# Optimization experiments

Measured on AMD Instinct MI355X. Metric: run time of the kernel, lower is better.

Reference implementation:

```python
import jax, jax.numpy as jnp
import numpy as np

H, DK = 16, 64
F = H * DK  # n_feat = 1024
B, T = 2, 2048


def setup_inputs() -> dict:
    key = jax.random.key(0)
    ks = jax.random.split(key, 11)
    mk = lambda k, sh: jax.random.normal(k, sh, dtype=jnp.float32)
    inp = {
        "query": mk(ks[0], (B, T, F)),
        "key": mk(ks[1], (B, T, F)),
        "value": mk(ks[2], (B, T, F)),
    }
    # Standard RoPE frequency table, shaped [T,1,1,DK] to broadcast over [t,b,h,d].
    pos = jnp.arange(T, dtype=jnp.float32)[:, None]
    inv_freq = 1.0 / (10000.0 ** (jnp.arange(0, DK, 2, dtype=jnp.float32) / DK))
    ang = pos * inv_freq                       # [T, DK/2]
    emb = jnp.concatenate([ang, ang], axis=-1)  # [T, DK]
    inp["cos"] = jnp.cos(emb)[:, None, None, :]
    inp["sin"] = jnp.sin(emb)[:, None, None, :]
    scale = 1.0 / np.sqrt(F).astype(np.float32)
    for i, n in enumerate(["wq", "wk", "wv", "wo"]):
        inp[n] = mk(ks[3 + i], (F, F)) * scale  # torch Linear weight layout [out,in]
    for i, n in enumerate(["bq", "bk", "bv", "bo"]):
        inp[n] = mk(ks[7 + i], (F,)) * 0.01
    return inp


def _rtt_half(x):
    d = x.shape[-1]
    return jnp.concatenate([-x[..., d // 2:], x[..., :d // 2]], axis=-1)


def reference(query, key, value, cos, sin, wq, bq, wk, bk, wv, bv, wo, bo):
    b, t, f = query.shape
    h, d = H, DK
    # [b,t,f] -> [t,b,h,d] as in the torch code (RoPE applied pre-projection)
    to_tbhd = lambda x: jnp.swapaxes(x, 0, 1).reshape(t, b, h, d)
    q = to_tbhd(query)
    k = to_tbhd(key)
    c, s = cos[:t], sin[:t]
    q = q * c + _rtt_half(q) * s
    k = k * c + _rtt_half(k) * s
    back = lambda x: jnp.swapaxes(x.reshape(t, b, f), 0, 1)  # -> [b,t,f]
    q, k = back(q), back(k)
    lin = lambda x, w, bias: x @ w.T + bias
    Q = lin(q, wq, bq).reshape(b, t, h, d)
    K = lin(k, wk, bk).reshape(b, t, h, d)
    V = lin(value, wv, bv).reshape(b, t, h, d)
    scores = jnp.einsum('bqhd,bkhd->bhqk', Q, K) / jnp.sqrt(jnp.float32(d))
    attn = jax.nn.softmax(scores, axis=-1)
    o = jnp.einsum('bhqk,bkhd->bqhd', attn, V).reshape(b, t, f)
    return o @ wo.T + bo
```

## Files before the change

kernel.cpp:

```cpp
#include <hip/hip_runtime.h>
#include <hip/hip_bf16.h>

#define DEVI __device__ __forceinline__

typedef unsigned short u16;
typedef unsigned int u32;
typedef __attribute__((ext_vector_type(8))) short bf16x8;
typedef __attribute__((ext_vector_type(4))) short bf16x4;
typedef __attribute__((ext_vector_type(4))) float f32x4;

#define Bn 2
#define Tn 2048
#define Hn 16
#define Dn 64
#define Fn 1024

DEVI u16 tobf(float f) {
    __hip_bfloat16 h = __float2bfloat16(f);
    return __builtin_bit_cast(u16, h);
}
DEVI float frombf(u16 u) {
    return __builtin_bit_cast(float, ((u32)u) << 16);
}

DEVI f32x4 mfma16(bf16x8 a, bf16x8 b, f32x4 c) {
    return __builtin_amdgcn_mfma_f32_16x16x32_bf16(a, b, c, 0, 0, 0);
}

DEVI void gload_lds16(const u16* g, u16* l) {
    __builtin_amdgcn_global_load_lds(
        (const __attribute__((address_space(1))) void*)g,
        (__attribute__((address_space(3))) void*)l, 16, 0, 0);
}

__global__ __launch_bounds__(256) void k_prep(const float* __restrict__ q,
                                              const float* __restrict__ k,
                                              const float* __restrict__ v,
                                              const float* __restrict__ cosb,
                                              const float* __restrict__ sinb,
                                              const float* __restrict__ wq,
                                              const float* __restrict__ wk,
                                              const float* __restrict__ wv,
                                              const float* __restrict__ wo,
                                              u16* __restrict__ Aq,
                                              u16* __restrict__ Ak,
                                              u16* __restrict__ Av) {
    if (blockIdx.x < 4096) {
        unsigned idx = blockIdx.x * 256 + threadIdx.x;
        unsigned which = idx >> 19;
        unsigned r = idx & 0x7FFFFu;
        unsigned d0 = (r & 7u) << 2;
        unsigned h = (r >> 3) & 15u;
        unsigned t = (r >> 7) & 2047u;
        unsigned b = (r >> 18) & 1u;
        const float* src = which ? k : q;
        u16* dst = which ? Ak : Aq;
        size_t base = ((size_t)(b * Tn + t)) * Fn + h * Dn;
        float4 lo = *(const float4*)(src + base + d0);
        float4 hi = *(const float4*)(src + base + d0 + 32);
        float4 cl = *(const float4*)(cosb + (size_t)t * Dn + d0);
        float4 ch = *(const float4*)(cosb + (size_t)t * Dn + d0 + 32);
        float4 sl = *(const float4*)(sinb + (size_t)t * Dn + d0);
        float4 sh = *(const float4*)(sinb + (size_t)t * Dn + d0 + 32);
        bf16x4 olo, ohi;
        olo[0] = (short)tobf(lo.x * cl.x - hi.x * sl.x);
        olo[1] = (short)tobf(lo.y * cl.y - hi.y * sl.y);
        olo[2] = (short)tobf(lo.z * cl.z - hi.z * sl.z);
        olo[3] = (short)tobf(lo.w * cl.w - hi.w * sl.w);
        ohi[0] = (short)tobf(hi.x * ch.x + lo.x * sh.x);
        ohi[1] = (short)tobf(hi.y * ch.y + lo.y * sh.y);
        ohi[2] = (short)tobf(hi.z * ch.z + lo.z * sh.z);
        ohi[3] = (short)tobf(hi.w * ch.w + lo.w * sh.w);
        *(bf16x4*)(dst + base + d0) = olo;
        *(bf16x4*)(dst + base + d0 + 32) = ohi;
    } else {
        size_t i8 = (((size_t)blockIdx.x - 4096) * 256 + threadIdx.x) * 8;
        const size_t M4 = (size_t)4 << 20, M1 = (size_t)1 << 20;
        const float* src;
        size_t off;
        if (i8 < M4)              { src = v;  off = i8; }
        else if (i8 < M4 + M1)    { src = wq; off = i8 - M4; }
        else if (i8 < M4 + 2*M1)  { src = wk; off = i8 - M4 - M1; }
        else if (i8 < M4 + 3*M1)  { src = wv; off = i8 - M4 - 2*M1; }
        else                      { src = wo; off = i8 - M4 - 3*M1; }
        float4 a = *(const float4*)(src + off);
        float4 c = *(const float4*)(src + off + 4);
        bf16x8 vv;
        vv[0] = (short)tobf(a.x); vv[1] = (short)tobf(a.y);
        vv[2] = (short)tobf(a.z); vv[3] = (short)tobf(a.w);
        vv[4] = (short)tobf(c.x); vv[5] = (short)tobf(c.y);
        vv[6] = (short)tobf(c.z); vv[7] = (short)tobf(c.w);
        *(bf16x8*)(Av + i8) = vv;
    }
}

DEVI void store_out(u16* p, float v) { *p = tobf(v); }
DEVI void store_out(float* p, float v) { *p = v; }

template <typename OUT>
DEVI void gemm_body(const u16* __restrict__ A, const u16* __restrict__ W,
                    const float* __restrict__ bias, OUT* __restrict__ C,
                    float scale, u16* As, u16* Bs, int mode) {
    const int tid = threadIdx.x;
    const int lane = tid & 63;
    const int wave = tid >> 6;
    const int l15 = lane & 15, l4 = lane >> 4;
    const int id = blockIdx.x + (blockIdx.y << 3);
    const int swz = ((id & 7) << 5) + (id >> 3);
    const int bn = (swz & 7) << 7, bm = (swz >> 3) << 7;
    const int wr = (wave >> 1) << 6, wc = (wave & 1) << 6;

    const int c0 = tid, c1 = tid + 256;
    const u16* A0p = A + (size_t)(bm + (c0 >> 2)) * 1024 + ((c0 & 3) << 3);
    const u16* A1p = A + (size_t)(bm + (c1 >> 2)) * 1024 + ((c1 & 3) << 3);
    const u16* B0p = W + (size_t)(bn + (c0 >> 2)) * 1024 + ((c0 & 3) << 3);
    const u16* B1p = W + (size_t)(bn + (c1 >> 2)) * 1024 + ((c1 & 3) << 3);
    u16* Ad0 = As + (c0 << 3);
    u16* Ad1 = As + (c1 << 3);
    u16* Bd0 = Bs + (c0 << 3);
    u16* Bd1 = Bs + (c1 << 3);

    f32x4 acc[4][4] = {};

    for (int k0 = 0; k0 < 1024; k0 += 32) {
        gload_lds16(A0p + k0, Ad0);
        gload_lds16(A1p + k0, Ad1);
        gload_lds16(B0p + k0, Bd0);
        gload_lds16(B1p + k0, Bd1);
        __syncthreads();
        bf16x8 af[4], bfr[4];
        #pragma unroll
        for (int m = 0; m < 4; m++)
            af[m] = *(const bf16x8*)(As + (wr + m * 16 + l15) * 32 + (l4 << 3));
        #pragma unroll
        for (int n = 0; n < 4; n++)
            bfr[n] = *(const bf16x8*)(Bs + (wc + n * 16 + l15) * 32 + (l4 << 3));
        #pragma unroll
        for (int m = 0; m < 4; m++)
            #pragma unroll
            for (int n = 0; n < 4; n++)
                acc[m][n] = mfma16(af[m], bfr[n], acc[m][n]);
        __syncthreads();
    }

    #pragma unroll
    for (int m = 0; m < 4; m++)
        #pragma unroll
        for (int n = 0; n < 4; n++) {
            const int gcol = bn + wc + n * 16 + l15;
            const float bb = bias[gcol];
            #pragma unroll
            for (int j = 0; j < 4; j++) {
                const int grow = bm + wr + m * 16 + (l4 << 2) + j;
                const float val = (acc[m][n][j] + bb) * scale;
                if (mode == 0) {
                    store_out(C + (size_t)grow * 1024 + gcol, val);
                } else {
                    const int b = grow >> 11, t = grow & 2047;
                    const int h = gcol >> 6, d = gcol & 63;
                    const int bh = b * 16 + h, tt2 = t >> 6, r = t & 63;
                    const size_t tbase = ((size_t)(bh * 32 + tt2)) << 12;
                    size_t off;
                    if (mode == 1) {
                        const int nn = ((r >> 5) << 1) | ((r >> 2) & 1);
                        const int kk = d >> 5, ll4 = (d >> 3) & 3, e = d & 7;
                        const int ll15 = (((r >> 3) & 3) << 2) | (r & 3);
                        off = tbase + ((size_t)(nn * 2 + kk) << 9) +
                              ((ll4 * 16 + ll15) << 3) + e;
                    } else {
                        const int kk = r >> 5, ll4 = (r >> 3) & 3, e = r & 7;
                        const int nd = d >> 4, ll15 = d & 15;
                        off = tbase + ((size_t)(kk * 4 + nd) << 9) +
                              ((ll4 * 16 + ll15) << 3) + e;
                    }
                    ((u16*)C)[off] = tobf(val);
                }
            }
        }
}

__global__ __launch_bounds__(256) void k_gemm_qkv(
    const u16* A0, const u16* W0, const float* b0, u16* C0,
    const u16* A1, const u16* W1, const float* b1, u16* C1,
    const u16* A2, const u16* W2, const float* b2, u16* C2) {
    __shared__ __align__(16) u16 As[128 * 32];
    __shared__ __align__(16) u16 Bs[128 * 32];
    const int z = blockIdx.z;
    const u16* A = z == 0 ? A0 : (z == 1 ? A1 : A2);
    const u16* W = z == 0 ? W0 : (z == 1 ? W1 : W2);
    const float* bias = z == 0 ? b0 : (z == 1 ? b1 : b2);
    u16* C = z == 0 ? C0 : (z == 1 ? C1 : C2);
    const float scale = z == 0 ? 0.125f * 1.4426950408889634f : 1.0f;
    gemm_body<u16>(A, W, bias, C, scale, As, Bs, z);
}

__global__ __launch_bounds__(256) void k_gemm_f32(const u16* __restrict__ A,
                                                  const u16* __restrict__ W,
                                                  const float* __restrict__ bias,
                                                  float* __restrict__ C) {
    __shared__ __align__(16) u16 As[128 * 32];
    __shared__ __align__(16) u16 Bs[128 * 32];
    gemm_body<float>(A, W, bias, C, 1.0f, As, Bs, 0);
}

__global__ __launch_bounds__(256) void k_attn(const u16* __restrict__ Qp,
                                              const u16* __restrict__ Kr,
                                              const u16* __restrict__ Vr,
                                              u16* __restrict__ Op0,
                                              u16* __restrict__ Op1,
                                              float* __restrict__ Ls) {
    __shared__ __align__(16) u16 Ks[2][4096];
    __shared__ __align__(16) u16 Vs[2][4096];
    const int tid = threadIdx.x, wave = tid >> 6, lane = tid & 63;
    const int l15 = lane & 15, l4 = lane >> 4;
    const int bh = blockIdx.x, b = bh >> 4, h = bh & 15;
    const int sp = blockIdx.z;
    const int q0 = blockIdx.y * 128 + wave * 32;
    const int tbase = sp << 4;

    bf16x8 aq[2][2];
    #pragma unroll
    for (int mq = 0; mq < 2; mq++)
        #pragma unroll
        for (int kk = 0; kk < 2; kk++)
            aq[mq][kk] = *(const bf16x8*)(Qp +
                ((size_t)(b * Tn + q0 + mq * 16 + l15)) * Fn + h * Dn + kk * 32 + (l4 << 3));

    f32x4 o[2][4] = {};
    f32x4 osum[2] = {};
    const f32x4 zero4 = {0.f, 0.f, 0.f, 0.f};

    bf16x8 ones;
    #pragma unroll
    for (int j = 0; j < 8; j++) ones[j] = (short)0x3F80;

    const u16* Kbr = Kr + ((size_t)bh << 17);
    const u16* Vbr = Vr + ((size_t)bh << 17);
    const int lo8 = lane * 8;

    #define STAGE(bf, tg)                                                     \
        _Pragma("unroll")                                                     \
        for (int i = 0; i < 2; i++) {                                         \
            const int c = wave + i * 4;                                       \
            gload_lds16(Kbr + (((tg) * 8 + c) << 9) + lo8,                    \
                        &Ks[bf][(c << 9) + lo8]);                             \
            gload_lds16(Vbr + (((tg) * 8 + c) << 9) + lo8,                    \
                        &Vs[bf][(c << 9) + lo8]);                             \
        }

    STAGE(0, tbase);
    __syncthreads();
    int cur = 0;

    #pragma unroll 1
    for (int tt = 0; tt < 16; tt++) {
        if (tt < 15) STAGE(cur ^ 1, tbase + tt + 1);

        bf16x8 ka[4][2], va[2][4];
        #pragma unroll
        for (int n = 0; n < 4; n++)
            #pragma unroll
            for (int kk = 0; kk < 2; kk++)
                ka[n][kk] = *(const bf16x8*)(&Ks[cur][((n * 2 + kk) << 9) + lo8]);
        #pragma unroll
        for (int kk = 0; kk < 2; kk++)
            #pragma unroll
            for (int nd = 0; nd < 4; nd++)
                va[kk][nd] = *(const bf16x8*)(&Vs[cur][((kk * 4 + nd) << 9) + lo8]);

        f32x4 s[2][4];
        __builtin_amdgcn_s_setprio(1);
        #pragma unroll
        for (int n = 0; n < 4; n++) {
            s[0][n] = mfma16(ka[n][0], aq[0][0], zero4);
            s[1][n] = mfma16(ka[n][0], aq[1][0], zero4);
            s[0][n] = mfma16(ka[n][1], aq[0][1], s[0][n]);
            s[1][n] = mfma16(ka[n][1], aq[1][1], s[1][n]);
        }
        __builtin_amdgcn_s_setprio(0);

        bf16x8 pb[2][2];
        #pragma unroll
        for (int mq = 0; mq < 2; mq++)
            #pragma unroll
            for (int kk = 0; kk < 2; kk++) {
                float p0 = __builtin_amdgcn_exp2f(s[mq][2 * kk][0]);
                float p1 = __builtin_amdgcn_exp2f(s[mq][2 * kk][1]);
                float p2 = __builtin_amdgcn_exp2f(s[mq][2 * kk][2]);
                float p3 = __builtin_amdgcn_exp2f(s[mq][2 * kk][3]);
                float p4 = __builtin_amdgcn_exp2f(s[mq][2 * kk + 1][0]);
                float p5 = __builtin_amdgcn_exp2f(s[mq][2 * kk + 1][1]);
                float p6 = __builtin_amdgcn_exp2f(s[mq][2 * kk + 1][2]);
                float p7 = __builtin_amdgcn_exp2f(s[mq][2 * kk + 1][3]);
                bf16x8 pv;
                pv[0] = (short)tobf(p0); pv[1] = (short)tobf(p1);
                pv[2] = (short)tobf(p2); pv[3] = (short)tobf(p3);
                pv[4] = (short)tobf(p4); pv[5] = (short)tobf(p5);
                pv[6] = (short)tobf(p6); pv[7] = (short)tobf(p7);
                pb[mq][kk] = pv;
            }

        __builtin_amdgcn_s_setprio(1);
        osum[0] = mfma16(ones, pb[0][0], osum[0]);
        osum[1] = mfma16(ones, pb[1][0], osum[1]);
        osum[0] = mfma16(ones, pb[0][1], osum[0]);
        osum[1] = mfma16(ones, pb[1][1], osum[1]);
        #pragma unroll
        for (int kk = 0; kk < 2; kk++)
            #pragma unroll
            for (int nd = 0; nd < 4; nd++) {
                o[0][nd] = mfma16(va[kk][nd], pb[0][kk], o[0][nd]);
                o[1][nd] = mfma16(va[kk][nd], pb[1][kk], o[1][nd]);
            }
        __builtin_amdgcn_s_setprio(0);

        __syncthreads();
        cur ^= 1;
    }
    #undef STAGE

    u16* OpS = sp ? Op1 : Op0;
    #pragma unroll
    for (int mq = 0; mq < 2; mq++) {
        const int q = q0 + mq * 16 + l15;
        const float lsum = osum[mq][0];
        float inv = 1.f / lsum;
        #pragma unroll
        for (int nd = 0; nd < 4; nd++) {
            bf16x4 ov;
            ov[0] = (short)tobf(o[mq][nd][0] * inv);
            ov[1] = (short)tobf(o[mq][nd][1] * inv);
            ov[2] = (short)tobf(o[mq][nd][2] * inv);
            ov[3] = (short)tobf(o[mq][nd][3] * inv);
            *(bf16x4*)(OpS + ((size_t)(b * Tn + q)) * Fn +
                       h * Dn + nd * 16 + (l4 << 2)) = ov;
        }
        if (l4 == 0)
            Ls[(((size_t)(sp * 2 + b)) * Tn + q) * Hn + h] = lsum;
    }
}

__global__ __launch_bounds__(256) void k_combine(const u16* __restrict__ Op0,
                                                 const u16* __restrict__ Op1,
                                                 const float* __restrict__ Ls,
                                                 u16* __restrict__ Oa) {
    size_t e0 = ((size_t)blockIdx.x * 256 + threadIdx.x) * 8;
    int row = (int)(e0 >> 10);
    int b = row >> 11, q = row & 2047;
    int h = (int)(e0 >> 6) & 15;
    float l0 = Ls[(((size_t)(0 + b)) * Tn + q) * Hn + h];
    float l1 = Ls[(((size_t)(2 + b)) * Tn + q) * Hn + h];
    float inv = 1.f / (l0 + l1);
    float w0 = l0 * inv, w1 = l1 * inv;
    bf16x8 x0 = *(const bf16x8*)(Op0 + e0);
    bf16x8 x1 = *(const bf16x8*)(Op1 + e0);
    bf16x8 out;
    #pragma unroll
    for (int j = 0; j < 8; j++)
        out[j] = (short)tobf(frombf((u16)x0[j]) * w0 + frombf((u16)x1[j]) * w1);
    *(bf16x8*)(Oa + e0) = out;
}

extern "C" void kernel_launch(void* const* d_in, const int* in_sizes, int n_in,
                              void* d_out, int out_size, void* d_ws, size_t ws_size,
                              hipStream_t stream) {
    const float* q    = (const float*)d_in[0];
    const float* k    = (const float*)d_in[1];
    const float* v    = (const float*)d_in[2];
    const float* cosb = (const float*)d_in[3];
    const float* sinb = (const float*)d_in[4];
    const float* wq   = (const float*)d_in[5];
    const float* wk   = (const float*)d_in[6];
    const float* wv   = (const float*)d_in[7];
    const float* wo   = (const float*)d_in[8];
    const float* bq   = (const float*)d_in[9];
    const float* bk   = (const float*)d_in[10];
    const float* bv   = (const float*)d_in[11];
    const float* bo   = (const float*)d_in[12];

    char* ws = (char*)d_ws;
    char* dob = (char*)d_out;
    const size_t MB = (size_t)1 << 20;
    u16* Aq  = (u16*)(ws);
    u16* Ak  = (u16*)(ws + 8 * MB);
    u16* Av  = (u16*)(ws + 16 * MB);
    u16* Wq  = (u16*)(ws + 24 * MB);
    u16* Wk  = (u16*)(ws + 26 * MB);
    u16* Wv  = (u16*)(ws + 28 * MB);
    u16* Wo  = (u16*)(ws + 30 * MB);
    u16* Qp  = (u16*)(ws + 32 * MB);
    u16* Kr  = (u16*)(ws + 40 * MB);
    u16* Vr  = (u16*)(ws + 48 * MB);
    u16* Op0 = (u16*)(dob);
    u16* Op1 = (u16*)(dob + 8 * MB);
    float* Ls = (float*)(ws + 16 * MB);
    u16* Oa  = (u16*)(ws);

    k_prep<<<8192, 256, 0, stream>>>(q, k, v, cosb, sinb, wq, wk, wv, wo,
                                     Aq, Ak, Av);
    k_gemm_qkv<<<dim3(8, 32, 3), 256, 0, stream>>>(Aq, Wq, bq, Qp,
                                                   Ak, Wk, bk, Kr,
                                                   Av, Wv, bv, Vr);
    k_attn<<<dim3(32, 16, 2), 256, 0, stream>>>(Qp, Kr, Vr, Op0, Op1, Ls);
    k_combine<<<2048, 256, 0, stream>>>(Op0, Op1, Ls, Oa);
    k_gemm_f32<<<dim3(8, 32), 256, 0, stream>>>(Oa, Wo, bo, (float*)d_out);
}
```

Measured before the change: 129.3 us.

## Double GEMM K-tile to 64 and store LDS in MFMA-fragment order

The projection GEMMs now load a 128x64 K-slice per iteration instead of 128x32, which halves the number of loop iterations and barrier pairs. The LDS layout is rearranged so each 16-row by 32-column fragment is stored contiguously in lane order, letting every wave read its MFMA operand with one linear 16-byte load per lane and avoiding bank conflicts from the old row-strided reads. LDS use per block doubles to 32 KB, which may lower occupancy, and there is still no double-buffering, so load latency is not overlapped with compute.

```diff
diff --git a/kernel.cpp b/kernel.cpp
--- a/kernel.cpp
+++ b/kernel.cpp
@@ -110,36 +110,44 @@
     const int bn = (swz & 7) << 7, bm = (swz >> 3) << 7;
     const int wr = (wave >> 1) << 6, wc = (wave & 1) << 6;
 
-    const int c0 = tid, c1 = tid + 256;
-    const u16* A0p = A + (size_t)(bm + (c0 >> 2)) * 1024 + ((c0 & 3) << 3);
-    const u16* A1p = A + (size_t)(bm + (c1 >> 2)) * 1024 + ((c1 & 3) << 3);
-    const u16* B0p = W + (size_t)(bn + (c0 >> 2)) * 1024 + ((c0 & 3) << 3);
-    const u16* B1p = W + (size_t)(bn + (c1 >> 2)) * 1024 + ((c1 & 3) << 3);
-    u16* Ad0 = As + (c0 << 3);
-    u16* Ad1 = As + (c1 << 3);
-    u16* Bd0 = Bs + (c0 << 3);
-    u16* Bd1 = Bs + (c1 << 3);
+    const u16* Ap[4];
+    const u16* Bp[4];
+    #pragma unroll
+    for (int i = 0; i < 4; i++) {
+        const int s = tid + (i << 8);
+        const int row = ((s >> 7) << 4) + (s & 15);
+        const int col = (((s >> 6) & 1) << 5) + (((s >> 4) & 3) << 3);
+        Ap[i] = A + (size_t)(bm + row) * 1024 + col;
+        Bp[i] = W + (size_t)(bn + row) * 1024 + col;
+    }
 
     f32x4 acc[4][4] = {};
 
-    for (int k0 = 0; k0 < 1024; k0 += 32) {
-        gload_lds16(A0p + k0, Ad0);
-        gload_lds16(A1p + k0, Ad1);
-        gload_lds16(B0p + k0, Bd0);
-        gload_lds16(B1p + k0, Bd1);
+    for (int k0 = 0; k0 < 1024; k0 += 64) {
+        #pragma unroll
+        for (int i = 0; i < 4; i++) {
+            const int s8 = (tid + (i << 8)) << 3;
+            gload_lds16(Ap[i] + k0, As + s8);
+            gload_lds16(Bp[i] + k0, Bs + s8);
+        }
         __syncthreads();
-        bf16x8 af[4], bfr[4];
-        #pragma unroll
-        for (int m = 0; m < 4; m++)
-            af[m] = *(const bf16x8*)(As + (wr + m * 16 + l15) * 32 + (l4 << 3));
-        #pragma unroll
-        for (int n = 0; n < 4; n++)
-            bfr[n] = *(const bf16x8*)(Bs + (wc + n * 16 + l15) * 32 + (l4 << 3));
-        #pragma unroll
-        for (int m = 0; m < 4; m++)
+        #pragma unroll
+        for (int kk = 0; kk < 2; kk++) {
+            bf16x8 af[4], bfr[4];
+            #pragma unroll
+            for (int m = 0; m < 4; m++)
+                af[m] = *(const bf16x8*)(As +
+                    (((((wr >> 4) + m) << 7) + (kk << 6) + lane) << 3));
             #pragma unroll
             for (int n = 0; n < 4; n++)
-                acc[m][n] = mfma16(af[m], bfr[n], acc[m][n]);
+                bfr[n] = *(const bf16x8*)(Bs +
+                    (((((wc >> 4) + n) << 7) + (kk << 6) + lane) << 3));
+            #pragma unroll
+            for (int m = 0; m < 4; m++)
+                #pragma unroll
+                for (int n = 0; n < 4; n++)
+                    acc[m][n] = mfma16(af[m], bfr[n], acc[m][n]);
+        }
         __syncthreads();
     }
 
@@ -183,8 +191,8 @@
     const u16* A0, const u16* W0, const float* b0, u16* C0,
     const u16* A1, const u16* W1, const float* b1, u16* C1,
     const u16* A2, const u16* W2, const float* b2, u16* C2) {
-    __shared__ __align__(16) u16 As[128 * 32];
-    __shared__ __align__(16) u16 Bs[128 * 32];
+    __shared__ __align__(16) u16 As[128 * 64];
+    __shared__ __align__(16) u16 Bs[128 * 64];
     const int z = blockIdx.z;
     const u16* A = z == 0 ? A0 : (z == 1 ? A1 : A2);
     const u16* W = z == 0 ? W0 : (z == 1 ? W1 : W2);
@@ -198,8 +206,8 @@
                                                   const u16* __restrict__ W,
                                                   const float* __restrict__ bias,
                                                   float* __restrict__ C) {
-    __shared__ __align__(16) u16 As[128 * 32];
-    __shared__ __align__(16) u16 Bs[128 * 32];
+    __shared__ __align__(16) u16 As[128 * 64];
+    __shared__ __align__(16) u16 Bs[128 * 64];
     gemm_body<float>(A, W, bias, C, 1.0f, As, Bs, 0);
 }
 
```

New measurement: 162.8 us. 1.26x slower.
